# Kernel optimization log

Measured on AMD Instinct MI355X. Metric: run time of the kernel, lower is better.

Reference implementation:

```python
import jax, jax.numpy as jnp
import numpy as np
from jax import lax

B, T, V, E, H, K = 64, 512, 30000, 256, 256, 9


def setup_inputs() -> dict:
    key = jax.random.key(0)
    ks = jax.random.split(key, 15)
    s = 0.08
    return {
        "word_inputs": jax.random.randint(ks[0], (B, T), 0, V),
        "word_seq_lengths": jax.random.randint(ks[1], (B,), 1, T + 1),
        "seq_token_label": jax.random.randint(ks[2], (B, T), 0, K),
        "word_vec": jax.random.normal(ks[3], (V, E), jnp.float32) * s,
        "W_ih_f": jax.random.normal(ks[4], (4 * H, E), jnp.float32) * s,
        "W_hh_f": jax.random.normal(ks[5], (4 * H, H), jnp.float32) * s,
        "b_f": jax.random.normal(ks[6], (4 * H,), jnp.float32) * s,
        "W_ih_b": jax.random.normal(ks[7], (4 * H, E), jnp.float32) * s,
        "W_hh_b": jax.random.normal(ks[8], (4 * H, H), jnp.float32) * s,
        "b_b": jax.random.normal(ks[9], (4 * H,), jnp.float32) * s,
        "W_out": jax.random.normal(ks[10], (K, 2 * H), jnp.float32) * s,
        "b_out": jax.random.normal(ks[11], (K,), jnp.float32) * s,
        "start_trans": jax.random.normal(ks[12], (K,), jnp.float32) * s,
        "end_trans": jax.random.normal(ks[13], (K,), jnp.float32) * s,
        "trans": jax.random.normal(ks[14], (K, K), jnp.float32) * s,
    }


def _lstm_dir(x, W_ih, W_hh, b):
    # x: [B,T,E] -> h: [B,T,H]; torch gate order (i, f, g, o)
    gx = jnp.einsum('bte,ge->btg', x, W_ih) + b  # input projection hoisted out of scan
    h0 = jnp.zeros((x.shape[0], W_hh.shape[1]), x.dtype)

    def step(carry, g_t):
        h, c = carry
        g = g_t + h @ W_hh.T
        i, f, gg, o = jnp.split(g, 4, axis=-1)
        c = jax.nn.sigmoid(f) * c + jax.nn.sigmoid(i) * jnp.tanh(gg)
        h = jax.nn.sigmoid(o) * jnp.tanh(c)
        return (h, c), h

    _, hs = lax.scan(step, (h0, h0), jnp.swapaxes(gx, 0, 1))
    return jnp.swapaxes(hs, 0, 1)


def reference(word_inputs, word_seq_lengths, seq_token_label, word_vec,
              W_ih_f, W_hh_f, b_f, W_ih_b, W_hh_b, b_b,
              W_out, b_out, start_trans, end_trans, trans):
    t_idx = jnp.arange(T)
    mask = t_idx[None, :] < word_seq_lengths[:, None]  # [B,T] bool (pack_padded semantics)
    # index map that reverses the valid prefix of each sequence (involution)
    rev_idx = jnp.where(mask, word_seq_lengths[:, None] - 1 - t_idx[None, :], t_idx[None, :])

    emb = word_vec[word_inputs]  # [B,T,E]
    h_fwd = _lstm_dir(emb, W_ih_f, W_hh_f, b_f)
    emb_rev = jnp.take_along_axis(emb, rev_idx[:, :, None], axis=1)
    h_bwd = jnp.take_along_axis(_lstm_dir(emb_rev, W_ih_b, W_hh_b, b_b), rev_idx[:, :, None], axis=1)
    feats = jnp.concatenate([h_fwd, h_bwd], axis=-1) * mask[:, :, None]  # [B,T,2H]
    emissions = feats @ W_out.T + b_out  # [B,T,K]

    mf = mask.astype(emissions.dtype)
    # ---- CRF numerator (score of gold path) ----
    emit_sc = jnp.take_along_axis(emissions, seq_token_label[:, :, None], 2)[:, :, 0]  # [B,T]
    num = start_trans[seq_token_label[:, 0]] + emit_sc[:, 0]
    trans_sc = trans[seq_token_label[:, :-1], seq_token_label[:, 1:]]  # [B,T-1]
    num = num + jnp.sum((trans_sc + emit_sc[:, 1:]) * mf[:, 1:], axis=1)
    last_tags = jnp.take_along_axis(seq_token_label, (word_seq_lengths - 1)[:, None], 1)[:, 0]
    num = num + end_trans[last_tags]

    # ---- CRF log-partition (alpha recursion) ----
    em_t = jnp.swapaxes(emissions[:, 1:], 0, 1)  # [T-1,B,K]
    mk_t = jnp.swapaxes(mask[:, 1:], 0, 1)       # [T-1,B]
    score0 = start_trans[None, :] + emissions[:, 0]  # [B,K]

    def alpha_step(score, inp):
        e_t, m_t = inp
        nxt = jax.nn.logsumexp(score[:, :, None] + trans[None], axis=1) + e_t
        return jnp.where(m_t[:, None], nxt, score), None

    scoreZ, _ = lax.scan(alpha_step, score0, (em_t, mk_t))
    denom = jax.nn.logsumexp(scoreZ + end_trans[None, :], axis=1)
    ner_loss = -jnp.mean(num - denom)  # reduction='mean' over batch, negated

    # ---- Viterbi decode ----
    def vit_step(score, inp):
        e_t, m_t = inp
        tot = score[:, :, None] + trans[None]  # [B,K,K]
        best_prev = jnp.argmax(tot, axis=1)    # [B,K]
        nxt = jnp.max(tot, axis=1) + e_t
        return jnp.where(m_t[:, None], nxt, score), best_prev

    scoreV, hist = lax.scan(vit_step, score0, (em_t, mk_t))  # hist [T-1,B,K]
    best_last = jnp.argmax(scoreV + end_trans[None, :], axis=1)  # [B]

    def back_step(cur, inp):
        h_t, m_t = inp
        new = jnp.take_along_axis(h_t, cur[:, None], 1)[:, 0]
        cur = jnp.where(m_t, new, cur)
        return cur, cur

    _, preds_rev = lax.scan(back_step, best_last, (hist[::-1], mk_t[::-1]))  # [T-1,B]
    preds = jnp.concatenate([jnp.swapaxes(preds_rev[::-1], 0, 1), best_last[:, None]], axis=1)  # [B,T]
    preds = jnp.where(mask, preds, 0)

    return ner_loss, preds, feats
```

## Files before the change

### kernel.cpp

```cpp
#include <hip/hip_runtime.h>
#include <hip/hip_bf16.h>
#include <math.h>

#ifndef __has_builtin
#define __has_builtin(x) 0
#endif

typedef unsigned int uint;
typedef unsigned short ushort;
typedef _Float16 half2_t __attribute__((ext_vector_type(2)));

#define WREG_UINTS (34 * 2 * 512)
#define WLDS_U4    (19 * 512)
#define WSTR_U4    (28 * 512)

__device__ __forceinline__ float sigm(float x) {
    return __fdividef(1.0f, 1.0f + __expf(-x));
}
__device__ __forceinline__ float tanh_fast(float x) {
    float sg = __fdividef(1.0f, 1.0f + __expf(-2.0f * x));
    return sg + sg - 1.0f;
}
__device__ __forceinline__ float dot2f(uint w, uint h, float acc) {
#if __has_builtin(__builtin_amdgcn_fdot2)
    return __builtin_amdgcn_fdot2(__builtin_bit_cast(half2_t, w),
                                  __builtin_bit_cast(half2_t, h), acc, false);
#else
    half2_t a = __builtin_bit_cast(half2_t, w);
    half2_t b = __builtin_bit_cast(half2_t, h);
    return acc + (float)a.x * (float)b.x + (float)a.y * (float)b.y;
#endif
}
__device__ __forceinline__ uint packh2(float a, float b) {
    ushort u0 = __builtin_bit_cast(ushort, (_Float16)a);
    ushort u1 = __builtin_bit_cast(ushort, (_Float16)b);
    return (uint)u0 | ((uint)u1 << 16);
}

#define R34(X) \
  X(0) X(1) X(2) X(3) X(4) X(5) X(6) X(7) \
  X(8) X(9) X(10) X(11) X(12) X(13) X(14) X(15) \
  X(16) X(17) X(18) X(19) X(20) X(21) X(22) X(23) \
  X(24) X(25) X(26) X(27) X(28) X(29) X(30) X(31) \
  X(32) X(33)

#define WDECL(m) uint wA##m, wB##m;
#define WLOAD(m) wA##m = wreg[(2 * (m)) * 512 + tid]; \
                 wB##m = wreg[(2 * (m) + 1) * 512 + tid];
#define WSTEP(m) { \
    uint hp = (uint)__builtin_amdgcn_readlane((int)r0, (m)); \
    aA = dot2f(wA##m, hp, aA); \
    aB = dot2f(wB##m, hp, aB); }
#define LSTEP(i) { \
    uint4 w4 = lw4[(i) * 512 + tid]; \
    uint hp0 = (uint)__builtin_amdgcn_readlane( \
        (int)((34 + 2 * (i)) < 64 ? r0 : r1), (34 + 2 * (i)) & 63); \
    uint hp1 = (uint)__builtin_amdgcn_readlane( \
        (int)((35 + 2 * (i)) < 64 ? r0 : r1), (35 + 2 * (i)) & 63); \
    aA = dot2f(w4.x, hp0, aA); \
    aB = dot2f(w4.y, hp0, aB); \
    aA = dot2f(w4.z, hp1, aA); \
    aB = dot2f(w4.w, hp1, aB); }
#define SISSUE(a, b, c, d, k0) { \
    a = wstr4[((k0) + 0) * 512 + tid]; \
    b = wstr4[((k0) + 1) * 512 + tid]; \
    c = wstr4[((k0) + 2) * 512 + tid]; \
    d = wstr4[((k0) + 3) * 512 + tid]; }
#define SPAIR(u, k) { \
    uint hp0 = (uint)__builtin_amdgcn_readlane((int)r1, 8 + 2 * (k)); \
    uint hp1 = (uint)__builtin_amdgcn_readlane((int)r1, 9 + 2 * (k)); \
    aA = dot2f(u.x, hp0, aA); \
    aB = dot2f(u.y, hp0, aB); \
    aA = dot2f(u.z, hp1, aA); \
    aB = dot2f(u.w, hp1, aB); }
#define SCONS(a, b, c, d, k0) \
    SPAIR(a, (k0) + 0) SPAIR(b, (k0) + 1) SPAIR(c, (k0) + 2) SPAIR(d, (k0) + 3)

__global__ __launch_bounds__(256) void zero_kernel(float* __restrict__ out,
                                                   const int* __restrict__ lens) {
    int bid = blockIdx.x;
    if (bid < 65536) {
        int g = bid * 256 + threadIdx.x;
        int row = g >> 9;
        int t = row & 511;
        int b = row >> 9;
        if (t >= lens[b]) out[32769 + g] = 0.0f;
    } else if (bid < 65536 + 128) {
        int p = (bid - 65536) * 256 + threadIdx.x;
        out[1 + p] = 0.0f;
    } else if (threadIdx.x == 0) {
        out[0] = 0.0f;
    }
}

__global__ __launch_bounds__(256) void pack_kernel(const float* __restrict__ WF,
                                                   const float* __restrict__ WB,
                                                   uint* __restrict__ wregF,
                                                   uint* __restrict__ wregB,
                                                   uint* __restrict__ wldsF,
                                                   uint* __restrict__ wldsB,
                                                   uint* __restrict__ wstrF,
                                                   uint* __restrict__ wstrB) {
    int id = blockIdx.x * 256 + threadIdx.x;
    const float* W = WF; uint* wr = wregF; uint* wl = wldsF; uint* wsp = wstrF;
    if (id >= 131072) { id -= 131072; W = WB; wr = wregB; wl = wldsB; wsp = wstrB; }
    int m = id >> 10;
    int r = id & 1023;
    int x = r >> 9;
    int tl = r & 511;
    int j = tl >> 1, s = tl & 1;
    int q = (s << 1) + x;
    const float* row = W + ((size_t)((q << 8) + j) << 8);
    uint pk = packh2(row[2 * m], row[2 * m + 1]);
    if (m < 34) {
        wr[((m << 1) + x) * 512 + tl] = pk;
    } else if (m < 72) {
        int mL = m - 34;
        wl[(((mL >> 1) << 9) + tl) * 4 + ((mL & 1) << 1) + x] = pk;
    } else {
        int mS = m - 72;
        wsp[(((mS >> 1) << 9) + tl) * 4 + ((mS & 1) << 1) + x] = pk;
    }
}

__global__ __launch_bounds__(256) void wih_pack_kernel(const float* __restrict__ WihF,
                                                       const float* __restrict__ WihB,
                                                       uint* __restrict__ w16F,
                                                       uint* __restrict__ w16B) {
    int id = blockIdx.x * 256 + threadIdx.x;
    const float* W = WihF; uint* dst = w16F;
    if (id >= 131072) { id -= 131072; W = WihB; dst = w16B; }
    int col = id >> 7;
    int p = id & 127;
    int perm = ((col & 3) << 8) + (col >> 2);
    const float* row = W + ((size_t)perm << 8);
    dst[(col << 7) + p] = packh2(row[2 * p], row[2 * p + 1]);
}

__global__ __launch_bounds__(256) void gemm_gx_kernel(const int* __restrict__ widx,
                                                      const int* __restrict__ lens,
                                                      const float* __restrict__ wvec,
                                                      const uint* __restrict__ wih16,
                                                      const float* __restrict__ bias,
                                                      _Float16* __restrict__ gx) {
    int row0 = blockIdx.x * 64;
    int b = row0 >> 9;
    int t0 = row0 & 511;
    if (t0 >= lens[b]) return;
    int n0 = blockIdx.y * 64;

    __shared__ __align__(16) uint As[16][68];
    __shared__ __align__(16) uint Bs[16][68];
    __shared__ int aoff[64];

    int tid = threadIdx.x;
    if (tid < 64) aoff[tid] = widx[row0 + tid] << 8;
    __syncthreads();

    float acc[4][4] = {};
    int tn = tid & 15, tm = tid >> 4;

    for (int k0p = 0; k0p < 128; k0p += 16) {
#pragma unroll
        for (int p = 0; p < 4; ++p) {
            int lin = p * 256 + tid;
            int kp = lin & 15, m = lin >> 4;
            const float2 av = *reinterpret_cast<const float2*>(
                &wvec[aoff[m] + ((k0p + kp) << 1)]);
            As[kp][m] = packh2(av.x, av.y);
            Bs[kp][m] = wih16[((n0 + m) << 7) + k0p + kp];
        }
        __syncthreads();
#pragma unroll
        for (int kp = 0; kp < 16; ++kp) {
            uint4 a4 = *reinterpret_cast<const uint4*>(&As[kp][tm * 4]);
            uint4 b4 = *reinterpret_cast<const uint4*>(&Bs[kp][tn * 4]);
            uint am[4] = {a4.x, a4.y, a4.z, a4.w};
            uint bn[4] = {b4.x, b4.y, b4.z, b4.w};
#pragma unroll
            for (int i = 0; i < 4; ++i)
#pragma unroll
                for (int j = 0; j < 4; ++j) acc[i][j] = dot2f(am[i], bn[j], acc[i][j]);
        }
        __syncthreads();
    }

#pragma unroll
    for (int i = 0; i < 4; ++i) {
        int row = row0 + tm * 4 + i;
        ushort u[4];
#pragma unroll
        for (int j = 0; j < 4; ++j) {
            int col = n0 + tn * 4 + j;
            int perm = ((col & 3) << 8) + (col >> 2);
            u[j] = __builtin_bit_cast(ushort, (_Float16)(acc[i][j] + bias[perm]));
        }
        uint2 st;
        st.x = (uint)u[0] | ((uint)u[1] << 16);
        st.y = (uint)u[2] | ((uint)u[3] << 16);
        *reinterpret_cast<uint2*>(&gx[row * 1024 + n0 + tn * 4]) = st;
    }
}

__global__ __launch_bounds__(512)
void lstm_kernel(const _Float16* __restrict__ gx0,
                 const _Float16* __restrict__ gx1,
                 const uint* __restrict__ wreg0,
                 const uint* __restrict__ wreg1,
                 const uint* __restrict__ wlds0,
                 const uint* __restrict__ wlds1,
                 const uint* __restrict__ wstr0,
                 const uint* __restrict__ wstr1,
                 const int* __restrict__ lens,
                 float* __restrict__ feats) {
    int dir = blockIdx.x & 1;
    int b = blockIdx.x >> 1;
    const uint* gxu = reinterpret_cast<const uint*>(dir ? gx1 : gx0) + ((size_t)(b << 9) << 9);
    const uint* wreg = dir ? wreg1 : wreg0;
    const uint4* wlds4 = reinterpret_cast<const uint4*>(dir ? wlds1 : wlds0);
    const uint4* wstr4 = reinterpret_cast<const uint4*>(dir ? wstr1 : wstr0);
    int len = lens[b];
    int tid = threadIdx.x;
    int lane = tid & 63;
    int sg = tid & 1;

    __shared__ __align__(16) uint4 lw4[WLDS_U4];
    __shared__ __align__(16) uint hpair[2][128];

    for (int i = tid; i < WLDS_U4; i += 512) lw4[i] = wlds4[i];

    R34(WDECL)
    R34(WLOAD)
    __syncthreads();

    float c = 0.0f;
    uint r0 = 0, r1 = 0;
    int pp = 0;

    int t0i = dir ? (len - 1) : 0;
    uint g = gxu[(t0i << 9) + tid];

    for (int tp = 0; tp < len; ++tp) {
        int t = dir ? (len - 1 - tp) : tp;
        int tnn = dir ? (len - 2 - tp) : (tp + 1);
        tnn = tnn < 0 ? 0 : (tnn >= len ? len - 1 : tnn);
        uint gnext = gxu[(tnn << 9) + tid];

        half2_t gv = __builtin_bit_cast(half2_t, g);
        float aA = (float)gv.x;
        float aB = (float)gv.y;

        uint4 sA0, sA1, sA2, sA3;
        uint4 sB0, sB1, sB2, sB3;

        SISSUE(sA0, sA1, sA2, sA3, 0)
        WSTEP(0)  WSTEP(1)  WSTEP(2)  WSTEP(3)  WSTEP(4)  WSTEP(5)
        WSTEP(6)  WSTEP(7)  WSTEP(8)  WSTEP(9)  WSTEP(10) WSTEP(11)
        WSTEP(12) WSTEP(13) WSTEP(14) WSTEP(15) WSTEP(16)
        SISSUE(sB0, sB1, sB2, sB3, 4)
        SCONS(sA0, sA1, sA2, sA3, 0)
        WSTEP(17) WSTEP(18) WSTEP(19) WSTEP(20) WSTEP(21) WSTEP(22)
        WSTEP(23) WSTEP(24) WSTEP(25) WSTEP(26) WSTEP(27) WSTEP(28)
        WSTEP(29) WSTEP(30) WSTEP(31) WSTEP(32) WSTEP(33)
        SISSUE(sA0, sA1, sA2, sA3, 8)
        SCONS(sB0, sB1, sB2, sB3, 4)
        LSTEP(0) LSTEP(1) LSTEP(2) LSTEP(3) LSTEP(4) LSTEP(5) LSTEP(6)
        SISSUE(sB0, sB1, sB2, sB3, 12)
        SCONS(sA0, sA1, sA2, sA3, 8)
        LSTEP(7) LSTEP(8) LSTEP(9) LSTEP(10) LSTEP(11) LSTEP(12)
        SISSUE(sA0, sA1, sA2, sA3, 16)
        SCONS(sB0, sB1, sB2, sB3, 12)
        LSTEP(13) LSTEP(14) LSTEP(15) LSTEP(16) LSTEP(17) LSTEP(18)
        SISSUE(sB0, sB1, sB2, sB3, 20)
        SCONS(sA0, sA1, sA2, sA3, 16)
        SISSUE(sA0, sA1, sA2, sA3, 24)
        SCONS(sB0, sB1, sB2, sB3, 20)
        SCONS(sA0, sA1, sA2, sA3, 24)

        float y = sg ? aA + aA : aA;
        float sgm = __fdividef(1.0f, 1.0f + __expf(-y));
        float pA = sg ? sgm + sgm - 1.0f : sgm;
        float pB = sigm(aB);

        float oA = __shfl_xor(pA, 1);
        float oB = __shfl_xor(pB, 1);
        float si = sg ? oA : pA;
        float sf = sg ? oB : pB;
        float tg = sg ? pA : oA;
        float so = sg ? pB : oB;

        c = sf * c + si * tg;
        float h = so * tanh_fast(c);

        if (!sg) {
            reinterpret_cast<ushort*>(hpair[pp])[tid >> 1] =
                __builtin_bit_cast(ushort, (_Float16)h);
        }
        __syncthreads();
        if (!sg) {
            feats[(size_t)(((b << 9) + t)) * 512 + (dir << 8) + (tid >> 1)] = h;
        }
        r0 = hpair[pp][lane];
        r1 = hpair[pp][64 + lane];
        pp ^= 1;
        g = gnext;
    }
}

__global__ __launch_bounds__(64) void emis_kernel(const float* __restrict__ feats,
                                                  const float* __restrict__ Wout,
                                                  const float* __restrict__ bout,
                                                  const int* __restrict__ lens,
                                                  float* __restrict__ emis) {
    int r = blockIdx.x;
    int b = r >> 9, t = r & 511;
    if (t >= lens[b]) return;
    int lane = threadIdx.x;
    const float* fr = feats + (size_t)r * 512;
    float f[8];
#pragma unroll
    for (int i = 0; i < 8; ++i) f[i] = fr[i * 64 + lane];
#pragma unroll
    for (int k = 0; k < 9; ++k) {
        float p = 0.0f;
#pragma unroll
        for (int i = 0; i < 8; ++i) p = fmaf(f[i], Wout[k * 512 + i * 64 + lane], p);
#pragma unroll
        for (int off = 32; off; off >>= 1) p += __shfl_down(p, off);
        if (lane == 0) emis[r * 9 + k] = p + bout[k];
    }
}

__global__ __launch_bounds__(64) void crf_kernel(const float* __restrict__ emis,
                                                 const int* __restrict__ lens,
                                                 const int* __restrict__ labels,
                                                 const float* __restrict__ start_trans,
                                                 const float* __restrict__ end_trans,
                                                 const float* __restrict__ trans,
                                                 float* __restrict__ out) {
    int b = blockIdx.x;
    int len = lens[b];
    int lane = threadIdx.x;
    __shared__ float alpha[9], vit[9];
    __shared__ unsigned char hist[512 * 9];
    const float* eb = emis + b * 512 * 9;
    const int* lb = labels + b * 512;

    float tr[9];
    if (lane < 9) {
#pragma unroll
        for (int i = 0; i < 9; ++i) tr[i] = trans[i * 9 + lane];
        float s0 = start_trans[lane] + eb[lane];
        alpha[lane] = s0;
        vit[lane] = s0;
    }
    __syncthreads();

    for (int t = 1; t < len; ++t) {
        float na = 0.0f, nv = 0.0f;
        if (lane < 9) {
            float e = eb[t * 9 + lane];
            float a[9];
#pragma unroll
            for (int i = 0; i < 9; ++i) a[i] = alpha[i] + tr[i];
            float m = a[0];
#pragma unroll
            for (int i = 1; i < 9; ++i) m = fmaxf(m, a[i]);
            float s = 0.0f;
#pragma unroll
            for (int i = 0; i < 9; ++i) s += __expf(a[i] - m);
            na = m + __logf(s) + e;
            float bv = vit[0] + tr[0];
            int bi = 0;
#pragma unroll
            for (int i = 1; i < 9; ++i) {
                float x = vit[i] + tr[i];
                if (x > bv) { bv = x; bi = i; }
            }
            nv = bv + e;
            hist[t * 9 + lane] = (unsigned char)bi;
        }
        __syncthreads();
        if (lane < 9) { alpha[lane] = na; vit[lane] = nv; }
        __syncthreads();
    }

    float part = 0.0f;
    for (int t = 1 + lane; t < len; t += 64) {
        int yp = lb[t - 1], y = lb[t];
        part += trans[yp * 9 + y] + eb[t * 9 + y];
    }
#pragma unroll
    for (int off = 32; off; off >>= 1) part += __shfl_down(part, off);

    if (lane == 0) {
        int y0 = lb[0];
        float num = start_trans[y0] + eb[y0] + part + end_trans[lb[len - 1]];
        float m = alpha[0] + end_trans[0];
        for (int j = 1; j < 9; ++j) m = fmaxf(m, alpha[j] + end_trans[j]);
        float s = 0.0f;
        for (int j = 0; j < 9; ++j) s += __expf(alpha[j] + end_trans[j] - m);
        float denom = m + __logf(s);
        atomicAdd(out, (denom - num) * (1.0f / 64.0f));

        float bm = vit[0] + end_trans[0];
        int cur = 0;
        for (int j = 1; j < 9; ++j) {
            float x = vit[j] + end_trans[j];
            if (x > bm) { bm = x; cur = j; }
        }
        float* preds = out + 1 + b * 512;
        preds[len - 1] = (float)cur;
        for (int t = len - 1; t >= 1; --t) {
            cur = hist[t * 9 + cur];
            preds[t - 1] = (float)cur;
        }
    }
}

extern "C" void kernel_launch(void* const* d_in, const int* in_sizes, int n_in,
                              void* d_out, int out_size, void* d_ws, size_t ws_size,
                              hipStream_t stream) {
    const int* widx = (const int*)d_in[0];
    const int* lens = (const int*)d_in[1];
    const int* labels = (const int*)d_in[2];
    const float* wvec = (const float*)d_in[3];
    const float* WihF = (const float*)d_in[4];
    const float* WhhF = (const float*)d_in[5];
    const float* bF = (const float*)d_in[6];
    const float* WihB = (const float*)d_in[7];
    const float* WhhB = (const float*)d_in[8];
    const float* bB = (const float*)d_in[9];
    const float* Wout = (const float*)d_in[10];
    const float* bout = (const float*)d_in[11];
    const float* start_trans = (const float*)d_in[12];
    const float* end_trans = (const float*)d_in[13];
    const float* trans9 = (const float*)d_in[14];
    float* out = (float*)d_out;
    char* ws = (char*)d_ws;

    _Float16* gxF = (_Float16*)(ws);
    _Float16* gxB = (_Float16*)(ws + 67108864);
    uint* wregF   = (uint*)(ws + 134217728);
    uint* wregB   = (uint*)(ws + 134356992);
    uint* wldsF   = (uint*)(ws + 134496256);
    uint* wldsB   = (uint*)(ws + 134651904);
    uint* wstrF   = (uint*)(ws + 134807552);
    uint* wstrB   = (uint*)(ws + 135036928);
    uint* wih16F  = (uint*)(ws + 135266304);
    uint* wih16B  = (uint*)(ws + 135790592);
    float* emis   = (float*)(ws + 135266304);
    (void)in_sizes; (void)n_in; (void)out_size; (void)ws_size;

    float* feats = out + 1 + 32768;

    zero_kernel<<<65665, 256, 0, stream>>>(out, lens);
    pack_kernel<<<1024, 256, 0, stream>>>(WhhF, WhhB, wregF, wregB, wldsF, wldsB,
                                          wstrF, wstrB);
    wih_pack_kernel<<<1024, 256, 0, stream>>>(WihF, WihB, wih16F, wih16B);

    dim3 ggrid(512, 16);
    gemm_gx_kernel<<<ggrid, 256, 0, stream>>>(widx, lens, wvec, wih16F, bF, gxF);
    gemm_gx_kernel<<<ggrid, 256, 0, stream>>>(widx, lens, wvec, wih16B, bB, gxB);

    lstm_kernel<<<128, 512, 0, stream>>>(gxF, gxB, wregF, wregB, wldsF, wldsB,
                                         wstrF, wstrB, lens, feats);

    emis_kernel<<<32768, 64, 0, stream>>>(feats, Wout, bout, lens, emis);
    crf_kernel<<<64, 64, 0, stream>>>(emis, lens, labels, start_trans, end_trans, trans9, out);
}
```

Measured before the change: 1.640 ms.

## Rebalance LSTM recurrent weights toward streaming and software-pipeline weight loads

Shrinks the register-resident slice of W_hh from 34 to 26 k-pairs and grows the globally streamed slice from 28 to 32, keeping the LDS slice at 19 groups. LDS weight reads become a rotating three-buffer pipeline, and the first two streamed groups for the next timestep are issued before the barrier so their latency overlaps the synchronisation. The barrier becomes inline asm that waits only on lgkmcnt. The goal is lower register pressure and hidden memory latency on the serial recurrence, at the cost of more global weight traffic per step and a hand-written barrier that must stay correct.

```diff
diff --git a/kernel.cpp b/kernel.cpp
--- a/kernel.cpp
+++ b/kernel.cpp
@@ -10,9 +10,9 @@
 typedef unsigned short ushort;
 typedef _Float16 half2_t __attribute__((ext_vector_type(2)));
 
-#define WREG_UINTS (34 * 2 * 512)
+#define WREG_UINTS (26 * 2 * 512)
 #define WLDS_U4    (19 * 512)
-#define WSTR_U4    (28 * 512)
+#define WSTR_U4    (32 * 512)
 
 __device__ __forceinline__ float sigm(float x) {
     return __fdividef(1.0f, 1.0f + __expf(-x));
@@ -37,12 +37,11 @@
     return (uint)u0 | ((uint)u1 << 16);
 }
 
-#define R34(X) \
+#define R26(X) \
   X(0) X(1) X(2) X(3) X(4) X(5) X(6) X(7) \
   X(8) X(9) X(10) X(11) X(12) X(13) X(14) X(15) \
   X(16) X(17) X(18) X(19) X(20) X(21) X(22) X(23) \
-  X(24) X(25) X(26) X(27) X(28) X(29) X(30) X(31) \
-  X(32) X(33)
+  X(24) X(25)
 
 #define WDECL(m) uint wA##m, wB##m;
 #define WLOAD(m) wA##m = wreg[(2 * (m)) * 512 + tid]; \
@@ -51,30 +50,31 @@
     uint hp = (uint)__builtin_amdgcn_readlane((int)r0, (m)); \
     aA = dot2f(wA##m, hp, aA); \
     aB = dot2f(wB##m, hp, aB); }
-#define LSTEP(i) { \
-    uint4 w4 = lw4[(i) * 512 + tid]; \
-    uint hp0 = (uint)__builtin_amdgcn_readlane( \
-        (int)((34 + 2 * (i)) < 64 ? r0 : r1), (34 + 2 * (i)) & 63); \
-    uint hp1 = (uint)__builtin_amdgcn_readlane( \
-        (int)((35 + 2 * (i)) < 64 ? r0 : r1), (35 + 2 * (i)) & 63); \
-    aA = dot2f(w4.x, hp0, aA); \
-    aB = dot2f(w4.y, hp0, aB); \
-    aA = dot2f(w4.z, hp1, aA); \
-    aB = dot2f(w4.w, hp1, aB); }
-#define SISSUE(a, b, c, d, k0) { \
-    a = wstr4[((k0) + 0) * 512 + tid]; \
-    b = wstr4[((k0) + 1) * 512 + tid]; \
-    c = wstr4[((k0) + 2) * 512 + tid]; \
-    d = wstr4[((k0) + 3) * 512 + tid]; }
-#define SPAIR(u, k) { \
-    uint hp0 = (uint)__builtin_amdgcn_readlane((int)r1, 8 + 2 * (k)); \
-    uint hp1 = (uint)__builtin_amdgcn_readlane((int)r1, 9 + 2 * (k)); \
+
+#define LLOAD(dv, i) dv = lw4[(i) * 512 + tid];
+#define LCONS(dv, i) { \
+    uint hp0 = (uint)__builtin_amdgcn_readlane((int)r0, 26 + 2 * (i)); \
+    uint hp1 = (uint)__builtin_amdgcn_readlane((int)r0, 27 + 2 * (i)); \
+    aA = dot2f(dv.x, hp0, aA); \
+    aB = dot2f(dv.y, hp0, aB); \
+    aA = dot2f(dv.z, hp1, aA); \
+    aB = dot2f(dv.w, hp1, aB); }
+
+#define SGRP(u, s) { \
+    uint hp0 = (uint)__builtin_amdgcn_readlane((int)r1, 2 * (s)); \
+    uint hp1 = (uint)__builtin_amdgcn_readlane((int)r1, 2 * (s) + 1); \
     aA = dot2f(u.x, hp0, aA); \
     aB = dot2f(u.y, hp0, aB); \
     aA = dot2f(u.z, hp1, aA); \
     aB = dot2f(u.w, hp1, aB); }
-#define SCONS(a, b, c, d, k0) \
-    SPAIR(a, (k0) + 0) SPAIR(b, (k0) + 1) SPAIR(c, (k0) + 2) SPAIR(d, (k0) + 3)
+#define SISSUE(s0_, s1_, s2_, s3_, j) { \
+    s0_ = wstr4[(4 * (j) + 0) * 512 + tid]; \
+    s1_ = wstr4[(4 * (j) + 1) * 512 + tid]; \
+    s2_ = wstr4[(4 * (j) + 2) * 512 + tid]; \
+    s3_ = wstr4[(4 * (j) + 3) * 512 + tid]; }
+#define SCONSB(s0_, s1_, s2_, s3_, j) \
+    SGRP(s0_, 4 * (j) + 0) SGRP(s1_, 4 * (j) + 1) \
+    SGRP(s2_, 4 * (j) + 2) SGRP(s3_, 4 * (j) + 3)
 
 __global__ __launch_bounds__(256) void zero_kernel(float* __restrict__ out,
                                                    const int* __restrict__ lens) {
@@ -112,13 +112,13 @@
     int q = (s << 1) + x;
     const float* row = W + ((size_t)((q << 8) + j) << 8);
     uint pk = packh2(row[2 * m], row[2 * m + 1]);
-    if (m < 34) {
+    if (m < 26) {
         wr[((m << 1) + x) * 512 + tl] = pk;
-    } else if (m < 72) {
-        int mL = m - 34;
+    } else if (m < 64) {
+        int mL = m - 26;
         wl[(((mL >> 1) << 9) + tl) * 4 + ((mL & 1) << 1) + x] = pk;
     } else {
-        int mS = m - 72;
+        int mS = m - 64;
         wsp[(((mS >> 1) << 9) + tl) * 4 + ((mS & 1) << 1) + x] = pk;
     }
 }
@@ -229,8 +229,8 @@
 
     for (int i = tid; i < WLDS_U4; i += 512) lw4[i] = wlds4[i];
 
-    R34(WDECL)
-    R34(WLOAD)
+    R26(WDECL)
+    R26(WLOAD)
     __syncthreads();
 
     float c = 0.0f;
@@ -239,6 +239,13 @@
 
     int t0i = dir ? (len - 1) : 0;
     uint g = gxu[(t0i << 9) + tid];
+
+    uint4 sA0, sA1, sA2, sA3;
+    uint4 sB0, sB1, sB2, sB3;
+    uint4 d0, d1, d2;
+
+    SISSUE(sA0, sA1, sA2, sA3, 0)
+    SISSUE(sB0, sB1, sB2, sB3, 1)
 
     for (int tp = 0; tp < len; ++tp) {
         int t = dir ? (len - 1 - tp) : tp;
@@ -250,32 +257,45 @@
         float aA = (float)gv.x;
         float aB = (float)gv.y;
 
-        uint4 sA0, sA1, sA2, sA3;
-        uint4 sB0, sB1, sB2, sB3;
-
-        SISSUE(sA0, sA1, sA2, sA3, 0)
+        LLOAD(d0, 0) LLOAD(d1, 1)
         WSTEP(0)  WSTEP(1)  WSTEP(2)  WSTEP(3)  WSTEP(4)  WSTEP(5)
         WSTEP(6)  WSTEP(7)  WSTEP(8)  WSTEP(9)  WSTEP(10) WSTEP(11)
-        WSTEP(12) WSTEP(13) WSTEP(14) WSTEP(15) WSTEP(16)
-        SISSUE(sB0, sB1, sB2, sB3, 4)
-        SCONS(sA0, sA1, sA2, sA3, 0)
-        WSTEP(17) WSTEP(18) WSTEP(19) WSTEP(20) WSTEP(21) WSTEP(22)
-        WSTEP(23) WSTEP(24) WSTEP(25) WSTEP(26) WSTEP(27) WSTEP(28)
-        WSTEP(29) WSTEP(30) WSTEP(31) WSTEP(32) WSTEP(33)
-        SISSUE(sA0, sA1, sA2, sA3, 8)
-        SCONS(sB0, sB1, sB2, sB3, 4)
-        LSTEP(0) LSTEP(1) LSTEP(2) LSTEP(3) LSTEP(4) LSTEP(5) LSTEP(6)
-        SISSUE(sB0, sB1, sB2, sB3, 12)
-        SCONS(sA0, sA1, sA2, sA3, 8)
-        LSTEP(7) LSTEP(8) LSTEP(9) LSTEP(10) LSTEP(11) LSTEP(12)
-        SISSUE(sA0, sA1, sA2, sA3, 16)
-        SCONS(sB0, sB1, sB2, sB3, 12)
-        LSTEP(13) LSTEP(14) LSTEP(15) LSTEP(16) LSTEP(17) LSTEP(18)
-        SISSUE(sB0, sB1, sB2, sB3, 20)
-        SCONS(sA0, sA1, sA2, sA3, 16)
-        SISSUE(sA0, sA1, sA2, sA3, 24)
-        SCONS(sB0, sB1, sB2, sB3, 20)
-        SCONS(sA0, sA1, sA2, sA3, 24)
+        WSTEP(12)
+        SCONSB(sA0, sA1, sA2, sA3, 0)
+        SISSUE(sA0, sA1, sA2, sA3, 2)
+        WSTEP(13) WSTEP(14) WSTEP(15) WSTEP(16) WSTEP(17) WSTEP(18)
+        WSTEP(19) WSTEP(20) WSTEP(21) WSTEP(22) WSTEP(23) WSTEP(24)
+        WSTEP(25)
+        SCONSB(sB0, sB1, sB2, sB3, 1)
+        SISSUE(sB0, sB1, sB2, sB3, 3)
+        LLOAD(d2, 2)  LCONS(d0, 0)
+        LLOAD(d0, 3)  LCONS(d1, 1)
+        LLOAD(d1, 4)  LCONS(d2, 2)
+        LLOAD(d2, 5)  LCONS(d0, 3)
+        LLOAD(d0, 6)  LCONS(d1, 4)
+        SCONSB(sA0, sA1, sA2, sA3, 2)
+        SISSUE(sA0, sA1, sA2, sA3, 4)
+        LLOAD(d1, 7)  LCONS(d2, 5)
+        LLOAD(d2, 8)  LCONS(d0, 6)
+        LLOAD(d0, 9)  LCONS(d1, 7)
+        LLOAD(d1, 10) LCONS(d2, 8)
+        LLOAD(d2, 11) LCONS(d0, 9)
+        SCONSB(sB0, sB1, sB2, sB3, 3)
+        SISSUE(sB0, sB1, sB2, sB3, 5)
+        LLOAD(d0, 12) LCONS(d1, 10)
+        LLOAD(d1, 13) LCONS(d2, 11)
+        LLOAD(d2, 14) LCONS(d0, 12)
+        LLOAD(d0, 15) LCONS(d1, 13)
+        LLOAD(d1, 16) LCONS(d2, 14)
+        SCONSB(sA0, sA1, sA2, sA3, 4)
+        SISSUE(sA0, sA1, sA2, sA3, 6)
+        LLOAD(d2, 17) LCONS(d0, 15)
+        LLOAD(d0, 18) LCONS(d1, 16)
+        LCONS(d2, 17) LCONS(d0, 18)
+        SCONSB(sB0, sB1, sB2, sB3, 5)
+        SISSUE(sB0, sB1, sB2, sB3, 7)
+        SCONSB(sA0, sA1, sA2, sA3, 6)
+        SCONSB(sB0, sB1, sB2, sB3, 7)
 
         float y = sg ? aA + aA : aA;
         float sgm = __fdividef(1.0f, 1.0f + __expf(-y));
@@ -296,7 +316,9 @@
             reinterpret_cast<ushort*>(hpair[pp])[tid >> 1] =
                 __builtin_bit_cast(ushort, (_Float16)h);
         }
-        __syncthreads();
+        SISSUE(sA0, sA1, sA2, sA3, 0)
+        SISSUE(sB0, sB1, sB2, sB3, 1)
+        asm volatile("s_waitcnt lgkmcnt(0)\n\ts_barrier" ::: "memory");
         if (!sg) {
             feats[(size_t)(((b << 9) + t)) * 512 + (dir << 8) + (tid >> 1)] = h;
         }
@@ -442,11 +464,11 @@
     _Float16* gxF = (_Float16*)(ws);
     _Float16* gxB = (_Float16*)(ws + 67108864);
     uint* wregF   = (uint*)(ws + 134217728);
-    uint* wregB   = (uint*)(ws + 134356992);
-    uint* wldsF   = (uint*)(ws + 134496256);
-    uint* wldsB   = (uint*)(ws + 134651904);
-    uint* wstrF   = (uint*)(ws + 134807552);
-    uint* wstrB   = (uint*)(ws + 135036928);
+    uint* wregB   = (uint*)(ws + 134324224);
+    uint* wldsF   = (uint*)(ws + 134430720);
+    uint* wldsB   = (uint*)(ws + 134586368);
+    uint* wstrF   = (uint*)(ws + 134742016);
+    uint* wstrB   = (uint*)(ws + 135004160);
     uint* wih16F  = (uint*)(ws + 135266304);
     uint* wih16B  = (uint*)(ws + 135790592);
     float* emis   = (float*)(ws + 135266304);
```

Measured after the change: 1.621 ms. Within noise of the previous version (-1.1%).

## Store LDS and streamed recurrent weights as 8-bit fp8-e5 to cut per-step traffic

Applied to the files above, without the earlier changes.

Recurrent W_hh columns held in LDS and streamed from global memory are now packed as truncated 8-bit values (the top byte of fp16) and expanded back with byte-permute before fdot2. This lets more of the weight matrix fit in LDS and shrinks the streamed global portion from 28 to 6 uint4 rows per thread. The register-resident share drops from 34 to 28 pairs. Streamed loads for the next step are issued before the barrier, and the barrier is a raw s_barrier that waits only on lgkmcnt. The trade-off is much lower weight precision (about 2 mantissa bits), which may exceed tolerance, plus extra perm instructions per multiply-add.

```diff
diff --git a/kernel.cpp b/kernel.cpp
--- a/kernel.cpp
+++ b/kernel.cpp
@@ -10,9 +10,9 @@
 typedef unsigned short ushort;
 typedef _Float16 half2_t __attribute__((ext_vector_type(2)));
 
-#define WREG_UINTS (34 * 2 * 512)
+#define WREG_UINTS (28 * 2 * 512)
 #define WLDS_U4    (19 * 512)
-#define WSTR_U4    (28 * 512)
+#define WSTR_U4    (6 * 512)
 
 __device__ __forceinline__ float sigm(float x) {
     return __fdividef(1.0f, 1.0f + __expf(-x));
@@ -36,13 +36,19 @@
     ushort u1 = __builtin_bit_cast(ushort, (_Float16)b);
     return (uint)u0 | ((uint)u1 << 16);
 }
-
-#define R34(X) \
+__device__ __forceinline__ ushort e5pair(float a, float b) {
+    uint ua = (uint)__builtin_bit_cast(ushort, (_Float16)a);
+    uint ub = (uint)__builtin_bit_cast(ushort, (_Float16)b);
+    uint ba = ((ua + 0x80u) >> 8) & 0xFFu;
+    uint bb = ((ub + 0x80u) >> 8) & 0xFFu;
+    return (ushort)(ba | (bb << 8));
+}
+
+#define R28(X) \
   X(0) X(1) X(2) X(3) X(4) X(5) X(6) X(7) \
   X(8) X(9) X(10) X(11) X(12) X(13) X(14) X(15) \
   X(16) X(17) X(18) X(19) X(20) X(21) X(22) X(23) \
-  X(24) X(25) X(26) X(27) X(28) X(29) X(30) X(31) \
-  X(32) X(33)
+  X(24) X(25) X(26) X(27)
 
 #define WDECL(m) uint wA##m, wB##m;
 #define WLOAD(m) wA##m = wreg[(2 * (m)) * 512 + tid]; \
@@ -51,30 +57,21 @@
     uint hp = (uint)__builtin_amdgcn_readlane((int)r0, (m)); \
     aA = dot2f(wA##m, hp, aA); \
     aB = dot2f(wB##m, hp, aB); }
-#define LSTEP(i) { \
-    uint4 w4 = lw4[(i) * 512 + tid]; \
-    uint hp0 = (uint)__builtin_amdgcn_readlane( \
-        (int)((34 + 2 * (i)) < 64 ? r0 : r1), (34 + 2 * (i)) & 63); \
-    uint hp1 = (uint)__builtin_amdgcn_readlane( \
-        (int)((35 + 2 * (i)) < 64 ? r0 : r1), (35 + 2 * (i)) & 63); \
-    aA = dot2f(w4.x, hp0, aA); \
-    aB = dot2f(w4.y, hp0, aB); \
-    aA = dot2f(w4.z, hp1, aA); \
-    aB = dot2f(w4.w, hp1, aB); }
-#define SISSUE(a, b, c, d, k0) { \
-    a = wstr4[((k0) + 0) * 512 + tid]; \
-    b = wstr4[((k0) + 1) * 512 + tid]; \
-    c = wstr4[((k0) + 2) * 512 + tid]; \
-    d = wstr4[((k0) + 3) * 512 + tid]; }
-#define SPAIR(u, k) { \
-    uint hp0 = (uint)__builtin_amdgcn_readlane((int)r1, 8 + 2 * (k)); \
-    uint hp1 = (uint)__builtin_amdgcn_readlane((int)r1, 9 + 2 * (k)); \
-    aA = dot2f(u.x, hp0, aA); \
-    aB = dot2f(u.y, hp0, aB); \
-    aA = dot2f(u.z, hp1, aA); \
-    aB = dot2f(u.w, hp1, aB); }
-#define SCONS(a, b, c, d, k0) \
-    SPAIR(a, (k0) + 0) SPAIR(b, (k0) + 1) SPAIR(c, (k0) + 2) SPAIR(d, (k0) + 3)
+
+#define LC1(u, p) { \
+    uint hp_ = (uint)__builtin_amdgcn_readlane((int)((p) < 64 ? r0 : r1), (p) & 63); \
+    uint wa_ = __builtin_amdgcn_perm((u), 0u, 0x05000400u); \
+    uint wb_ = __builtin_amdgcn_perm((u), 0u, 0x07000600u); \
+    aA = dot2f(wa_, hp_, aA); \
+    aB = dot2f(wb_, hp_, aB); }
+#define LCONS8(dv, i) \
+    LC1(dv.x, 28 + 4 * (i)) LC1(dv.y, 29 + 4 * (i)) \
+    LC1(dv.z, 30 + 4 * (i)) LC1(dv.w, 31 + 4 * (i))
+#define SCONS8(sv, g2) \
+    LC1(sv.x, 104 + 4 * (g2)) LC1(sv.y, 105 + 4 * (g2)) \
+    LC1(sv.z, 106 + 4 * (g2)) LC1(sv.w, 107 + 4 * (g2))
+#define LLOAD(dv, i) dv = lw4[(i) * 512 + tid];
+#define SISS(sv, g2) sv = wstr4[(g2) * 512 + tid];
 
 __global__ __launch_bounds__(256) void zero_kernel(float* __restrict__ out,
                                                    const int* __restrict__ lens) {
@@ -111,15 +108,19 @@
     int j = tl >> 1, s = tl & 1;
     int q = (s << 1) + x;
     const float* row = W + ((size_t)((q << 8) + j) << 8);
-    uint pk = packh2(row[2 * m], row[2 * m + 1]);
-    if (m < 34) {
-        wr[((m << 1) + x) * 512 + tl] = pk;
-    } else if (m < 72) {
-        int mL = m - 34;
-        wl[(((mL >> 1) << 9) + tl) * 4 + ((mL & 1) << 1) + x] = pk;
+    float w0 = row[2 * m], w1 = row[2 * m + 1];
+    if (m < 28) {
+        wr[((m << 1) + x) * 512 + tl] = packh2(w0, w1);
+    } else if (m < 104) {
+        int mL = m - 28;
+        int i = mL >> 2, c = mL & 3;
+        size_t uidx = ((size_t)(i * 512 + tl) << 2) + c;
+        reinterpret_cast<ushort*>(wl)[uidx * 2 + x] = e5pair(w0, w1);
     } else {
-        int mS = m - 72;
-        wsp[(((mS >> 1) << 9) + tl) * 4 + ((mS & 1) << 1) + x] = pk;
+        int mS = m - 104;
+        int g2 = mS >> 2, c = mS & 3;
+        size_t uidx = ((size_t)(g2 * 512 + tl) << 2) + c;
+        reinterpret_cast<ushort*>(wsp)[uidx * 2 + x] = e5pair(w0, w1);
     }
 }
 
@@ -229,8 +230,8 @@
 
     for (int i = tid; i < WLDS_U4; i += 512) lw4[i] = wlds4[i];
 
-    R34(WDECL)
-    R34(WLOAD)
+    R28(WDECL)
+    R28(WLOAD)
     __syncthreads();
 
     float c = 0.0f;
@@ -239,6 +240,11 @@
 
     int t0i = dir ? (len - 1) : 0;
     uint g = gxu[(t0i << 9) + tid];
+
+    uint4 s0, s1, s2, s3, s4, s5;
+    uint4 d0, d1, d2, d3, d4;
+
+    SISS(s0, 0) SISS(s1, 1) SISS(s2, 2) SISS(s3, 3) SISS(s4, 4) SISS(s5, 5)
 
     for (int tp = 0; tp < len; ++tp) {
         int t = dir ? (len - 1 - tp) : tp;
@@ -250,32 +256,37 @@
         float aA = (float)gv.x;
         float aB = (float)gv.y;
 
-        uint4 sA0, sA1, sA2, sA3;
-        uint4 sB0, sB1, sB2, sB3;
-
-        SISSUE(sA0, sA1, sA2, sA3, 0)
+        LLOAD(d0, 0) LLOAD(d1, 1) LLOAD(d2, 2) LLOAD(d3, 3) LLOAD(d4, 4)
         WSTEP(0)  WSTEP(1)  WSTEP(2)  WSTEP(3)  WSTEP(4)  WSTEP(5)
         WSTEP(6)  WSTEP(7)  WSTEP(8)  WSTEP(9)  WSTEP(10) WSTEP(11)
-        WSTEP(12) WSTEP(13) WSTEP(14) WSTEP(15) WSTEP(16)
-        SISSUE(sB0, sB1, sB2, sB3, 4)
-        SCONS(sA0, sA1, sA2, sA3, 0)
-        WSTEP(17) WSTEP(18) WSTEP(19) WSTEP(20) WSTEP(21) WSTEP(22)
-        WSTEP(23) WSTEP(24) WSTEP(25) WSTEP(26) WSTEP(27) WSTEP(28)
-        WSTEP(29) WSTEP(30) WSTEP(31) WSTEP(32) WSTEP(33)
-        SISSUE(sA0, sA1, sA2, sA3, 8)
-        SCONS(sB0, sB1, sB2, sB3, 4)
-        LSTEP(0) LSTEP(1) LSTEP(2) LSTEP(3) LSTEP(4) LSTEP(5) LSTEP(6)
-        SISSUE(sB0, sB1, sB2, sB3, 12)
-        SCONS(sA0, sA1, sA2, sA3, 8)
-        LSTEP(7) LSTEP(8) LSTEP(9) LSTEP(10) LSTEP(11) LSTEP(12)
-        SISSUE(sA0, sA1, sA2, sA3, 16)
-        SCONS(sB0, sB1, sB2, sB3, 12)
-        LSTEP(13) LSTEP(14) LSTEP(15) LSTEP(16) LSTEP(17) LSTEP(18)
-        SISSUE(sB0, sB1, sB2, sB3, 20)
-        SCONS(sA0, sA1, sA2, sA3, 16)
-        SISSUE(sA0, sA1, sA2, sA3, 24)
-        SCONS(sB0, sB1, sB2, sB3, 20)
-        SCONS(sA0, sA1, sA2, sA3, 24)
+        WSTEP(12) WSTEP(13)
+        SCONS8(s0, 0) SCONS8(s1, 1)
+        WSTEP(14) WSTEP(15) WSTEP(16) WSTEP(17) WSTEP(18) WSTEP(19)
+        WSTEP(20) WSTEP(21) WSTEP(22) WSTEP(23) WSTEP(24) WSTEP(25)
+        WSTEP(26) WSTEP(27)
+        LCONS8(d0, 0)  LLOAD(d0, 5)
+        LCONS8(d1, 1)  LLOAD(d1, 6)
+        LCONS8(d2, 2)  LLOAD(d2, 7)
+        SCONS8(s2, 2)
+        LCONS8(d3, 3)  LLOAD(d3, 8)
+        LCONS8(d4, 4)  LLOAD(d4, 9)
+        LCONS8(d0, 5)  LLOAD(d0, 10)
+        SCONS8(s3, 3)
+        LCONS8(d1, 6)  LLOAD(d1, 11)
+        LCONS8(d2, 7)  LLOAD(d2, 12)
+        LCONS8(d3, 8)  LLOAD(d3, 13)
+        SCONS8(s4, 4)
+        LCONS8(d4, 9)  LLOAD(d4, 14)
+        LCONS8(d0, 10) LLOAD(d0, 15)
+        LCONS8(d1, 11) LLOAD(d1, 16)
+        SCONS8(s5, 5)
+        LCONS8(d2, 12) LLOAD(d2, 17)
+        LCONS8(d3, 13) LLOAD(d3, 18)
+        LCONS8(d4, 14)
+        LCONS8(d0, 15)
+        LCONS8(d1, 16)
+        LCONS8(d2, 17)
+        LCONS8(d3, 18)
 
         float y = sg ? aA + aA : aA;
         float sgm = __fdividef(1.0f, 1.0f + __expf(-y));
@@ -296,7 +307,8 @@
             reinterpret_cast<ushort*>(hpair[pp])[tid >> 1] =
                 __builtin_bit_cast(ushort, (_Float16)h);
         }
-        __syncthreads();
+        SISS(s0, 0) SISS(s1, 1) SISS(s2, 2) SISS(s3, 3) SISS(s4, 4) SISS(s5, 5)
+        asm volatile("s_waitcnt lgkmcnt(0)\n\ts_barrier" ::: "memory");
         if (!sg) {
             feats[(size_t)(((b << 9) + t)) * 512 + (dir << 8) + (tid >> 1)] = h;
         }
@@ -442,14 +454,14 @@
     _Float16* gxF = (_Float16*)(ws);
     _Float16* gxB = (_Float16*)(ws + 67108864);
     uint* wregF   = (uint*)(ws + 134217728);
-    uint* wregB   = (uint*)(ws + 134356992);
-    uint* wldsF   = (uint*)(ws + 134496256);
-    uint* wldsB   = (uint*)(ws + 134651904);
-    uint* wstrF   = (uint*)(ws + 134807552);
-    uint* wstrB   = (uint*)(ws + 135036928);
-    uint* wih16F  = (uint*)(ws + 135266304);
-    uint* wih16B  = (uint*)(ws + 135790592);
-    float* emis   = (float*)(ws + 135266304);
+    uint* wregB   = (uint*)(ws + 134332416);
+    uint* wldsF   = (uint*)(ws + 134447104);
+    uint* wldsB   = (uint*)(ws + 134602752);
+    uint* wstrF   = (uint*)(ws + 134758400);
+    uint* wstrB   = (uint*)(ws + 134807552);
+    uint* wih16F  = (uint*)(ws + 134856704);
+    uint* wih16B  = (uint*)(ws + 135380992);
+    float* emis   = (float*)(ws + 134856704);
     (void)in_sizes; (void)n_in; (void)out_size; (void)ws_size;
 
     float* feats = out + 1 + 32768;
```

New measurement: 1.879 ms. +14.6%, slower.
